# Kernel optimization log

Measured on AMD Instinct MI355X. Metric: run time of the kernel, lower is better.

## Reference

```python
import jax, jax.numpy as jnp
import numpy as np

B, H, D = 2, 16, 64
M = N = 4096
WM = WN = 64
R = 3
NEG = -10000.0


def _rand_blocks(m, n, wm, wn, r, last_idx):
    # Faithful port of bigbird_block_rand_mask (numpy RNG, seeded by caller).
    nb = m // wm
    rand = np.zeros((nb - 2, r), dtype=np.int32)
    mid = np.arange(1, n // wn - 1, dtype=np.int32)
    last = n // wn - 1
    if last_idx > 2 * wn:
        last = last_idx // wn - 1
    for i in range(1, nb - 1):
        start, end = i - 2, i
        if i == 1:
            rand[i - 1] = np.random.permutation(mid[2:last])[:r]
        elif i == 2:
            rand[i - 1] = np.random.permutation(mid[3:last])[:r]
        elif i == nb - 3 or i == nb - 2:
            rand[i - 1] = np.random.permutation(mid[:last])[:r]
        elif start > last:
            rand[i - 1] = np.random.permutation(mid[:last])[:r]
        elif end + 1 == last:
            rand[i - 1] = np.random.permutation(mid[:start])[:r]
        else:
            rand[i - 1] = np.random.permutation(np.concatenate((mid[:start], mid[end + 1:last])))[:r]
    return rand


def setup_inputs() -> dict:
    key = jax.random.key(0)
    kq, kk, kv = jax.random.split(key, 3)
    nb = M // WM
    q = jax.random.normal(kq, (B, H, M, D), jnp.float32)
    k = jax.random.normal(kk, (B, H, N, D), jnp.float32)
    v = jax.random.normal(kv, (B, H, N, D), jnp.float32)
    band_mask = jnp.ones((B, 1, nb - 4, WM, 3 * WN), jnp.float32)
    from_mask = jnp.ones((B, 1, M, 1), jnp.float32)
    to_mask = jnp.ones((B, 1, 1, N), jnp.float32)
    from_blocked_mask = jnp.ones((B, nb, WM), jnp.float32)
    to_blocked_mask = jnp.ones((B, nb, WN), jnp.float32)
    np.random.seed(0)
    ra = np.stack([_rand_blocks(M, N, WM, WN, R, 1024)[:nb - 2] for _ in range(H)], 0)
    rand_attn = jnp.asarray(np.broadcast_to(ra[None], (B, H, nb - 2, R)).copy(), jnp.int32)
    return dict(query_layer=q, key_layer=k, value_layer=v, band_mask=band_mask,
                from_mask=from_mask, to_mask=to_mask,
                from_blocked_mask=from_blocked_mask, to_blocked_mask=to_blocked_mask,
                rand_attn=rand_attn, batch_size=B, from_seq_length=M, to_seq_length=N)


def _forward(q, k, v, band_mask, from_mask, to_mask, from_blocked_mask, to_blocked_mask, rand_attn):
    b, h, m, d = q.shape
    n = k.shape[2]
    wm, wn, r = WM, WN, R
    nb = m // wm
    scale = 1.0 / np.sqrt(d)
    bq = q.reshape(b, h, nb, wm, d)
    bk = k.reshape(b, h, nb, wn, d)
    bv = v.reshape(b, h, nb, wn, d)

    # gather random key/value blocks: [b,h,nb-2,r*wn,d]
    idx = jnp.broadcast_to(rand_attn.reshape(b, h, (nb - 2) * r, 1, 1).astype(jnp.int32),
                           (b, h, (nb - 2) * r, wn, d))
    gk = jnp.take_along_axis(bk, idx, axis=2).reshape(b, h, nb - 2, r * wn, d)
    gv = jnp.take_along_axis(bv, idx, axis=2).reshape(b, h, nb - 2, r * wn, d)

    # random-block attention mask: [b,h,nb-2,wm,r*wn]
    bidx = jnp.arange(b)[:, None, None, None]
    rm = to_blocked_mask[bidx, rand_attn].reshape(b, h, nb - 2, r * wn)
    rand_mask = jnp.einsum('blq,bhlk->bhlqk', from_blocked_mask[:, 1:-1], rm)

    # --- first row-block: full attention over all keys ---
    p0 = jnp.einsum('bhqd,bhkd->bhqk', bq[:, :, 0], k) * scale + (1.0 - to_mask) * NEG
    c0 = jnp.einsum('bhqk,bhkd->bhqd', jax.nn.softmax(p0, -1), v)[:, :, None]

    # --- second row-block: blocks 0,1,2,last + random ---
    k1c = jnp.concatenate([bk[:, :, 0], bk[:, :, 1], bk[:, :, 2], bk[:, :, -1], gk[:, :, 0]], axis=2)
    v1c = jnp.concatenate([bv[:, :, 0], bv[:, :, 1], bv[:, :, 2], bv[:, :, -1], gv[:, :, 0]], axis=2)
    p1 = jnp.einsum('bhqd,bhkd->bhqk', bq[:, :, 1], k1c) * scale
    seq_pad = jnp.concatenate([to_mask[:, :, :, :3 * wn], to_mask[:, :, :, -wn:],
                               jnp.ones((b, 1, 1, r * wn), to_mask.dtype)], axis=3)
    rpad = jnp.concatenate([jnp.ones((b, h, wm, 4 * wn), rand_mask.dtype), rand_mask[:, :, 0]], axis=3)
    p1 = p1 + (1.0 - jnp.minimum(seq_pad, rpad)) * NEG
    c1 = jnp.einsum('bhqk,bhkd->bhqd', jax.nn.softmax(p1, -1), v1c)[:, :, None]

    # --- middle row-blocks: sliding window (3 blocks) + first + last + random ---
    ek = jnp.concatenate([bk[:, :, 1:-3], bk[:, :, 2:-2], bk[:, :, 3:-1]], axis=3)  # [b,h,nb-4,3wn,d]
    ev = jnp.concatenate([bv[:, :, 1:-3], bv[:, :, 2:-2], bv[:, :, 3:-1]], axis=3)
    mq = bq[:, :, 2:-2]
    inner = jnp.einsum('bhlqd,bhlkd->bhlqk', mq, ek) * scale + (1.0 - band_mask) * NEG
    randp = jnp.einsum('bhlqd,bhlkd->bhlqk', mq, gk[:, :, 1:-1]) * scale + (1.0 - rand_mask[:, :, 1:-1]) * NEG
    firstp = jnp.einsum('bhlqd,bhkd->bhlqk', mq, bk[:, :, 0]) * scale \
        + (1.0 - to_mask[:, :, :, :wn][:, :, :, None, :]) * NEG
    lastp = jnp.einsum('bhlqd,bhkd->bhlqk', mq, bk[:, :, -1]) * scale \
        + (1.0 - to_mask[:, :, :, -wn:][:, :, :, None, :]) * NEG
    band = jnp.concatenate([firstp, inner, randp, lastp], axis=-1)  # [b,h,nb-4,wm,(5+r)*wn]
    attn = jax.nn.softmax(band, -1)
    cmid = (jnp.einsum('bhlqk,bhlkd->bhlqd', attn[..., wn:4 * wn], ev)
            + jnp.einsum('bhlqk,bhlkd->bhlqd', attn[..., 4 * wn:4 * wn + r * wn], gv[:, :, 1:-1])
            + jnp.einsum('bhlqk,bhkd->bhlqd', attn[..., :wn], bv[:, :, 0])
            + jnp.einsum('bhlqk,bhkd->bhlqd', attn[..., -wn:], bv[:, :, -1]))

    # --- second-to-last row-block: blocks 0,-3,-2,-1 + random ---
    k2c = jnp.concatenate([bk[:, :, 0], bk[:, :, -3], bk[:, :, -2], bk[:, :, -1], gk[:, :, -1]], axis=2)
    v2c = jnp.concatenate([bv[:, :, 0], bv[:, :, -3], bv[:, :, -2], bv[:, :, -1], gv[:, :, -1]], axis=2)
    p2 = jnp.einsum('bhqd,bhkd->bhqk', bq[:, :, -2], k2c) * scale
    seq_pad2 = jnp.concatenate([to_mask[:, :, :, :wn], to_mask[:, :, :, -3 * wn:],
                                jnp.ones((b, 1, 1, r * wn), to_mask.dtype)], axis=3)
    rpad2 = jnp.concatenate([jnp.ones((b, h, wm, 4 * wn), rand_mask.dtype), rand_mask[:, :, -1]], axis=3)
    p2 = p2 + (1.0 - jnp.minimum(seq_pad2, rpad2)) * NEG
    c2 = jnp.einsum('bhqk,bhkd->bhqd', jax.nn.softmax(p2, -1), v2c)[:, :, None]

    # --- last row-block: full attention ---
    p3 = jnp.einsum('bhqd,bhkd->bhqk', bq[:, :, -1], k) * scale + (1.0 - to_mask) * NEG
    c3 = jnp.einsum('bhqk,bhkd->bhqd', jax.nn.softmax(p3, -1), v)[:, :, None]

    ctx = jnp.concatenate([c0, c1, cmid, c2, c3], axis=2).reshape(b, h, m, d) * from_mask
    return jnp.transpose(ctx, (0, 2, 1, 3))  # [b, m, h, d]


def reference(query_layer, key_layer, value_layer, band_mask, from_mask, to_mask,
              from_blocked_mask, to_blocked_mask, rand_attn,
              batch_size, from_seq_length, to_seq_length):
    return _forward(query_layer, key_layer, value_layer, band_mask, from_mask, to_mask,
                    from_blocked_mask, to_blocked_mask, rand_attn)
```

## Files before the change

kernel.cpp:

```cpp
#include <hip/hip_runtime.h>
#include <math.h>

constexpr int B_  = 2;
constexpr int H_  = 16;
constexpr int M_  = 4096;
constexpr int NB_ = 64;
constexpr int R_  = 3;
constexpr float LOG2E  = 1.44269504089f;
constexpr float SCALE2 = 0.125f * LOG2E;
constexpr float NEG2   = -10000.0f * LOG2E;

constexpr int PER_BH = 62 + 16;
constexpr int NWG    = B_ * H_ * PER_BH;
constexpr int PACC_OFF = 0;
constexpr int PM_OFF   = B_ * H_ * 2 * 8 * 64 * 64;
constexpr int PL_OFF   = PM_OFF + B_ * H_ * 2 * 8 * 64;

typedef short bf16x8 __attribute__((ext_vector_type(8)));
typedef float f32x4  __attribute__((ext_vector_type(4)));

__device__ __forceinline__ short bf16s(float x) {
    return __builtin_bit_cast(short, (__bf16)x);
}
__device__ __forceinline__ unsigned pack_bf16(float a, float b) {
    unsigned short ul = __builtin_bit_cast(unsigned short, (__bf16)a);
    unsigned short uh = __builtin_bit_cast(unsigned short, (__bf16)b);
    return (unsigned)ul | ((unsigned)uh << 16);
}

__device__ __forceinline__ int tile_kb(int e, int ch, int qb, int ra0, int ra1, int ra2, int i) {
    if (e >= 0) return ch * 8 + i;
    const int rnd = (i == 4) ? ra0 : ((i == 5) ? ra1 : ra2);
    if (qb == 1)        return (i < 3) ? i : ((i == 3) ? NB_ - 1 : rnd);
    if (qb == NB_ - 2)  return (i == 0) ? 0 : ((i < 4) ? 60 + i : rnd);
    if (i == 0) return 0;
    if (i < 4)  return qb - 2 + i;
    if (i < 7)  return rnd;
    return NB_ - 1;
}

__device__ __forceinline__ int tile_mode(int e, int qb, int i, int& boff) {
    boff = 0;
    if (e >= 0) return 0;
    if (qb == 1 || qb == NB_ - 2) return (i >= 4) ? 2 : 0;
    if (i >= 1 && i < 4) { boff = (i - 1) * 64; return 1; }
    if (i >= 4 && i < 7) return 2;
    return 0;
}

__global__ __launch_bounds__(256, 4)
void bigbird_mfma(const float* __restrict__ q,  const float* __restrict__ k,
                  const float* __restrict__ v,  const float* __restrict__ band_mask,
                  const float* __restrict__ from_mask, const float* __restrict__ to_mask,
                  const float* __restrict__ from_blocked, const float* __restrict__ to_blocked,
                  const int*   __restrict__ rand_attn,   float* __restrict__ out,
                  float* __restrict__ ws)
{
    __shared__ int4 kf[2][8][64];
    __shared__ int4 vf[2][8][64];

    const int wg  = (blockIdx.x & 7) * (NWG / 8) + (blockIdx.x >> 3);
    const int bh  = wg / PER_BH;
    const int idx = wg % PER_BH;
    const int h   = bh % H_;
    const int b   = bh / H_;
    int qb, e = -1, ch = 0;
    if (idx < 62)      { qb = idx + 1; }
    else if (idx < 70) { e = 0; ch = idx - 62; qb = 0; }
    else               { e = 1; ch = idx - 70; qb = NB_ - 1; }

    const int t  = threadIdx.x;
    const int l  = t & 63;
    const int w  = t >> 6;
    const int c  = l & 15;
    const int hh = l >> 4;

    int ra0 = 0, ra1 = 0, ra2 = 0;
    int nkb;
    if (e >= 0) nkb = 8;
    else {
        const int* ra = rand_attn + ((b * H_ + h) * (NB_ - 2) + (qb - 1)) * R_;
        ra0 = ra[0]; ra1 = ra[1]; ra2 = ra[2];
        nkb = (qb == 1 || qb == NB_ - 2) ? 7 : 8;
    }

    const int rr  = t >> 2;
    const int cc4 = t & 3;
    const float* kbase = k + ((size_t)bh * M_ + rr) * 64 + cc4 * 16;
    const int kslot = (rr >> 4) * 2 + (cc4 >> 1);
    const int kr15  = rr & 15;
    const int kg0   = (cc4 & 1) * 2;

    const int d0v  = (t & 31) * 2;
    const int oct8 = t >> 5;
    const float* vbase = v + (size_t)bh * M_ * 64 + (size_t)(oct8 * 8) * 64 + d0v;
    const int vslot = (d0v >> 4) * 2 + (oct8 >> 2);
    const int vidx  = (oct8 & 3) * 16 + (d0v & 15);

    bf16x8 qf[2];
    {
        const float* qp = q + ((size_t)bh * M_ + (size_t)qb * 64 + w * 16 + c) * 64 + hh * 8;
        #pragma unroll
        for (int dh = 0; dh < 2; ++dh) {
            float4 a0 = *(const float4*)(qp + dh * 32);
            float4 a1 = *(const float4*)(qp + dh * 32 + 4);
            bf16x8 qv;
            qv[0] = bf16s(a0.x); qv[1] = bf16s(a0.y); qv[2] = bf16s(a0.z); qv[3] = bf16s(a0.w);
            qv[4] = bf16s(a1.x); qv[5] = bf16s(a1.y); qv[6] = bf16s(a1.z); qv[7] = bf16s(a1.w);
            qf[dh] = qv;
        }
    }

    const float fbv = from_blocked[(b * NB_ + qb) * 64 + (w * 16 + c)];

    float mrun = -INFINITY, lrun = 0.0f;
    f32x4 O[4];
    #pragma unroll
    for (int nf = 0; nf < 4; ++nf) { O[nf][0] = 0.f; O[nf][1] = 0.f; O[nf][2] = 0.f; O[nf][3] = 0.f; }

    float4 kr0, kr1, kr2, kr3;
    float2 vr[8];

    {
        const int kb0 = tile_kb(e, ch, qb, ra0, ra1, ra2, 0);
        const float4* kp4 = (const float4*)(kbase + (size_t)kb0 * 4096);
        kr0 = kp4[0]; kr1 = kp4[1]; kr2 = kp4[2]; kr3 = kp4[3];
        const float* vp = vbase + (size_t)kb0 * 4096;
        #pragma unroll
        for (int j = 0; j < 8; ++j) vr[j] = *(const float2*)(vp + j * 64);

        float kfl[16];
        kfl[0]=kr0.x; kfl[1]=kr0.y; kfl[2]=kr0.z; kfl[3]=kr0.w;
        kfl[4]=kr1.x; kfl[5]=kr1.y; kfl[6]=kr1.z; kfl[7]=kr1.w;
        kfl[8]=kr2.x; kfl[9]=kr2.y; kfl[10]=kr2.z; kfl[11]=kr2.w;
        kfl[12]=kr3.x; kfl[13]=kr3.y; kfl[14]=kr3.z; kfl[15]=kr3.w;
        bf16x8 o0, o1;
        #pragma unroll
        for (int j = 0; j < 8; ++j) { o0[j] = bf16s(kfl[j]); o1[j] = bf16s(kfl[8 + j]); }
        kf[0][kslot][kg0 * 16 + kr15]       = __builtin_bit_cast(int4, o0);
        kf[0][kslot][(kg0 + 1) * 16 + kr15] = __builtin_bit_cast(int4, o1);

        bf16x8 va, vb2;
        #pragma unroll
        for (int j = 0; j < 8; ++j) { va[j] = bf16s(vr[j].x); vb2[j] = bf16s(vr[j].y); }
        vf[0][vslot][vidx]     = __builtin_bit_cast(int4, va);
        vf[0][vslot][vidx + 1] = __builtin_bit_cast(int4, vb2);

        if (1 < nkb) {
            const int kb1 = tile_kb(e, ch, qb, ra0, ra1, ra2, 1);
            const float4* kn4 = (const float4*)(kbase + (size_t)kb1 * 4096);
            kr0 = kn4[0]; kr1 = kn4[1]; kr2 = kn4[2]; kr3 = kn4[3];
            const float* vn = vbase + (size_t)kb1 * 4096;
            #pragma unroll
            for (int j = 0; j < 8; ++j) vr[j] = *(const float2*)(vn + j * 64);
        }
    }
    __syncthreads();

    for (int it = 0; it < nkb; ++it) {
        const int cur = it & 1;
        const int kb = tile_kb(e, ch, qb, ra0, ra1, ra2, it);
        int boffC; const int modeC = tile_mode(e, qb, it, boffC);

        f32x4 sf[4];
        #pragma unroll
        for (int f = 0; f < 4; ++f) { sf[f][0]=0.f; sf[f][1]=0.f; sf[f][2]=0.f; sf[f][3]=0.f; }
        __builtin_amdgcn_s_setprio(1);
        #pragma unroll
        for (int f = 0; f < 4; ++f) {
            sf[f] = __builtin_amdgcn_mfma_f32_16x16x32_bf16(
                        __builtin_bit_cast(bf16x8, kf[cur][f * 2 + 0][l]), qf[0], sf[f], 0, 0, 0);
            sf[f] = __builtin_amdgcn_mfma_f32_16x16x32_bf16(
                        __builtin_bit_cast(bf16x8, kf[cur][f * 2 + 1][l]), qf[1], sf[f], 0, 0, 0);
        }
        __builtin_amdgcn_s_setprio(0);

        if (it + 1 < nkb) {
            const int nxt = cur ^ 1;
            float kfl[16];
            kfl[0]=kr0.x; kfl[1]=kr0.y; kfl[2]=kr0.z; kfl[3]=kr0.w;
            kfl[4]=kr1.x; kfl[5]=kr1.y; kfl[6]=kr1.z; kfl[7]=kr1.w;
            kfl[8]=kr2.x; kfl[9]=kr2.y; kfl[10]=kr2.z; kfl[11]=kr2.w;
            kfl[12]=kr3.x; kfl[13]=kr3.y; kfl[14]=kr3.z; kfl[15]=kr3.w;
            bf16x8 o0, o1;
            #pragma unroll
            for (int j = 0; j < 8; ++j) { o0[j] = bf16s(kfl[j]); o1[j] = bf16s(kfl[8 + j]); }
            kf[nxt][kslot][kg0 * 16 + kr15]       = __builtin_bit_cast(int4, o0);
            kf[nxt][kslot][(kg0 + 1) * 16 + kr15] = __builtin_bit_cast(int4, o1);

            bf16x8 va, vb2;
            #pragma unroll
            for (int j = 0; j < 8; ++j) { va[j] = bf16s(vr[j].x); vb2[j] = bf16s(vr[j].y); }
            vf[nxt][vslot][vidx]     = __builtin_bit_cast(int4, va);
            vf[nxt][vslot][vidx + 1] = __builtin_bit_cast(int4, vb2);
        }

        float msk[4][4];
        if (modeC == 0) {
            const float* mp = to_mask + b * M_ + kb * 64 + 4 * hh;
            #pragma unroll
            for (int f = 0; f < 4; ++f) {
                float4 mv = *(const float4*)(mp + 16 * f);
                msk[f][0] = mv.x; msk[f][1] = mv.y; msk[f][2] = mv.z; msk[f][3] = mv.w;
            }
        } else if (modeC == 1) {
            const float* mp = band_mask + (((size_t)b * (NB_ - 4) + (qb - 2)) * 64 + (w * 16 + c)) * 192 + boffC + 4 * hh;
            #pragma unroll
            for (int f = 0; f < 4; ++f) {
                float4 mv = *(const float4*)(mp + 16 * f);
                msk[f][0] = mv.x; msk[f][1] = mv.y; msk[f][2] = mv.z; msk[f][3] = mv.w;
            }
        } else {
            const float* mp = to_blocked + (b * NB_ + kb) * 64 + 4 * hh;
            #pragma unroll
            for (int f = 0; f < 4; ++f) {
                float4 mv = *(const float4*)(mp + 16 * f);
                msk[f][0] = fbv * mv.x; msk[f][1] = fbv * mv.y;
                msk[f][2] = fbv * mv.z; msk[f][3] = fbv * mv.w;
            }
        }

        if (it + 2 < nkb) {
            const int kb2 = tile_kb(e, ch, qb, ra0, ra1, ra2, it + 2);
            const float4* kp4 = (const float4*)(kbase + (size_t)kb2 * 4096);
            kr0 = kp4[0]; kr1 = kp4[1]; kr2 = kp4[2]; kr3 = kp4[3];
            const float* vp = vbase + (size_t)kb2 * 4096;
            #pragma unroll
            for (int j = 0; j < 8; ++j) vr[j] = *(const float2*)(vp + j * 64);
        }

        float p[4][4];
        float tmax = -INFINITY;
        #pragma unroll
        for (int f = 0; f < 4; ++f) {
            #pragma unroll
            for (int r = 0; r < 4; ++r) {
                const float s = sf[f][r] * SCALE2 + (1.0f - msk[f][r]) * NEG2;
                p[f][r] = s;
                tmax = fmaxf(tmax, s);
            }
        }
        tmax = fmaxf(tmax, __shfl_xor(tmax, 16));
        tmax = fmaxf(tmax, __shfl_xor(tmax, 32));
        const float mnew = fmaxf(mrun, tmax);
        const float fs = exp2f(mrun - mnew);
        float sum = 0.0f;
        #pragma unroll
        for (int f = 0; f < 4; ++f) {
            #pragma unroll
            for (int r = 0; r < 4; ++r) { p[f][r] = exp2f(p[f][r] - mnew); sum += p[f][r]; }
        }
        sum += __shfl_xor(sum, 16);
        sum += __shfl_xor(sum, 32);
        lrun = lrun * fs + sum;
        mrun = mnew;

        const float fr0 = __shfl(fs, hh * 4 + 0);
        const float fr1 = __shfl(fs, hh * 4 + 1);
        const float fr2 = __shfl(fs, hh * 4 + 2);
        const float fr3 = __shfl(fs, hh * 4 + 3);
        #pragma unroll
        for (int nf = 0; nf < 4; ++nf) {
            O[nf][0] *= fr0; O[nf][1] *= fr1; O[nf][2] *= fr2; O[nf][3] *= fr3;
        }

        unsigned pks[4][2];
        #pragma unroll
        for (int f = 0; f < 4; ++f) {
            pks[f][0] = pack_bf16(p[f][0], p[f][1]);
            pks[f][1] = pack_bf16(p[f][2], p[f][3]);
        }
        #pragma unroll
        for (int kh = 0; kh < 2; ++kh) {
            unsigned ad[4];
            #pragma unroll
            for (int wq = 0; wq < 4; ++wq) {
                const int pos = wq >> 1, ww = wq & 1;
                const int src = c + 16 * ((2 * hh + pos) & 3);
                const unsigned x = (unsigned)__shfl((int)pks[2 * kh][ww], src);
                const unsigned y = (unsigned)__shfl((int)pks[2 * kh + 1][ww], src);
                ad[wq] = (hh & 2) ? y : x;
            }
            const uint4 adv = make_uint4(ad[0], ad[1], ad[2], ad[3]);
            const bf16x8 pa = __builtin_bit_cast(bf16x8, adv);
            __builtin_amdgcn_s_setprio(1);
            #pragma unroll
            for (int nf = 0; nf < 4; ++nf) {
                O[nf] = __builtin_amdgcn_mfma_f32_16x16x32_bf16(
                            pa, __builtin_bit_cast(bf16x8, vf[cur][nf * 2 + kh][l]), O[nf], 0, 0, 0);
            }
            __builtin_amdgcn_s_setprio(0);
        }

        __syncthreads();
    }

    if (e < 0) {
        #pragma unroll
        for (int r = 0; r < 4; ++r) {
            const float lr  = __shfl(lrun, hh * 4 + r);
            const int   qg  = qb * 64 + w * 16 + hh * 4 + r;
            const float fmv = from_mask[b * M_ + qg];
            const float scl = fmv / lr;
            float* op = out + (((size_t)b * M_ + qg) * H_ + h) * 64 + c;
            #pragma unroll
            for (int nf = 0; nf < 4; ++nf) op[nf * 16] = O[nf][r] * scl;
        }
    } else {
        const int pe = (bh * 2 + e) * 8 + ch;
        #pragma unroll
        for (int r = 0; r < 4; ++r) {
            const int qlocal = w * 16 + hh * 4 + r;
            float* pa = ws + PACC_OFF + ((size_t)pe * 64 + qlocal) * 64 + c;
            #pragma unroll
            for (int nf = 0; nf < 4; ++nf) pa[nf * 16] = O[nf][r];
        }
        if (hh == 0) {
            ws[PM_OFF + pe * 64 + w * 16 + c] = mrun;
            ws[PL_OFF + pe * 64 + w * 16 + c] = lrun;
        }
    }
}

__global__ __launch_bounds__(256)
void bigbird_combine(const float* __restrict__ ws, const float* __restrict__ from_mask,
                     float* __restrict__ out)
{
    const int g  = blockIdx.x;
    const int e  = g & 1;
    const int bh = g >> 1;
    const int h  = bh % H_;
    const int b  = bh / H_;
    const int qb = e ? NB_ - 1 : 0;

    const int t  = threadIdx.x;
    const int r  = t >> 2;
    const int dq = (t & 3) * 16;

    float mc[8], lc[8];
    float m = -INFINITY;
    #pragma unroll
    for (int c = 0; c < 8; ++c) {
        mc[c] = ws[PM_OFF + (g * 8 + c) * 64 + r];
        lc[c] = ws[PL_OFF + (g * 8 + c) * 64 + r];
        m = fmaxf(m, mc[c]);
    }
    float l = 0.0f;
    float acc[16];
    #pragma unroll
    for (int j = 0; j < 16; ++j) acc[j] = 0.0f;
    #pragma unroll
    for (int c = 0; c < 8; ++c) {
        const float sc = exp2f(mc[c] - m);
        l += lc[c] * sc;
        const float4* pa = (const float4*)(ws + PACC_OFF + ((size_t)(g * 8 + c) * 64 + r) * 64 + dq);
        #pragma unroll
        for (int j4 = 0; j4 < 4; ++j4) {
            float4 av = pa[j4];
            acc[j4 * 4 + 0] += sc * av.x;
            acc[j4 * 4 + 1] += sc * av.y;
            acc[j4 * 4 + 2] += sc * av.z;
            acc[j4 * 4 + 3] += sc * av.w;
        }
    }
    const float fm = from_mask[b * M_ + qb * 64 + r];
    const float s  = fm / l;
    float* op = out + (((size_t)b * M_ + qb * 64 + r) * H_ + h) * 64 + dq;
    #pragma unroll
    for (int j4 = 0; j4 < 4; ++j4) {
        float4 o;
        o.x = acc[j4 * 4 + 0] * s; o.y = acc[j4 * 4 + 1] * s;
        o.z = acc[j4 * 4 + 2] * s; o.w = acc[j4 * 4 + 3] * s;
        *(float4*)(op + j4 * 4) = o;
    }
}

extern "C" void kernel_launch(void* const* d_in, const int* in_sizes, int n_in,
                              void* d_out, int out_size, void* d_ws, size_t ws_size,
                              hipStream_t stream) {
    const float* q  = (const float*)d_in[0];
    const float* k  = (const float*)d_in[1];
    const float* v  = (const float*)d_in[2];
    const float* bm = (const float*)d_in[3];
    const float* fm = (const float*)d_in[4];
    const float* tm = (const float*)d_in[5];
    const float* fb = (const float*)d_in[6];
    const float* tb = (const float*)d_in[7];
    const int*   ra = (const int*)d_in[8];
    float* o  = (float*)d_out;
    float* ws = (float*)d_ws;

    hipLaunchKernelGGL(bigbird_mfma, dim3(NWG), dim3(256), 0, stream,
                       q, k, v, bm, fm, tm, fb, tb, ra, o, ws);
    hipLaunchKernelGGL(bigbird_combine, dim3(B_ * H_ * 2), dim3(256), 0, stream,
                       ws, fm, o);
}
```

Before: 96.12 us.

## Pre-pack K/V into bf16 MFMA fragment layout and use single-wave strip kernel

Adds a prep kernel that converts K and V once into bf16 tiles already laid out as MFMA operand fragments in workspace. A new one-wave-per-16-row-strip attention kernel then loads those fragments straight from global memory into registers, with no LDS staging or workgroup barriers, across many more, smaller workgroups. This removes repeated per-block fp32-to-bf16 conversion and shared-memory traffic. In exchange it adds an extra launch and a workspace round trip for K/V, and each K/V tile is reloaded by the four strips that use it. The old kernel is kept as a fallback when the workspace is too small.

```diff
diff --git a/kernel.cpp b/kernel.cpp
--- a/kernel.cpp
+++ b/kernel.cpp
@@ -15,6 +15,12 @@
 constexpr int PACC_OFF = 0;
 constexpr int PM_OFF   = B_ * H_ * 2 * 8 * 64 * 64;
 constexpr int PL_OFF   = PM_OFF + B_ * H_ * 2 * 8 * 64;
+constexpr size_t KV_BYTE_OFF = (size_t)(PL_OFF + B_ * H_ * 2 * 8 * 64) * 4;
+constexpr size_t KV_BYTES    = (size_t)B_ * H_ * 64 * 1024 * 16;
+constexpr size_t WS_NEED     = KV_BYTE_OFF + KV_BYTES;
+
+constexpr int PER_BH1 = 312;
+constexpr int NWG1    = B_ * H_ * PER_BH1;
 
 typedef short bf16x8 __attribute__((ext_vector_type(8)));
 typedef float f32x4  __attribute__((ext_vector_type(4)));
@@ -46,6 +52,238 @@
     if (i >= 1 && i < 4) { boff = (i - 1) * 64; return 1; }
     if (i >= 4 && i < 7) return 2;
     return 0;
+}
+
+__global__ __launch_bounds__(256)
+void bigbird_prep(const float* __restrict__ k, const float* __restrict__ v,
+                  int4* __restrict__ wskv)
+{
+    __shared__ float kt[64][66];
+    __shared__ float vt[64][66];
+    const int g = blockIdx.x;
+    const int t = threadIdx.x;
+    const int row = t >> 2, cc = (t & 3) * 16;
+    const float* kp = k + (size_t)g * 4096 + row * 64 + cc;
+    const float* vp = v + (size_t)g * 4096 + row * 64 + cc;
+    #pragma unroll
+    for (int j4 = 0; j4 < 4; ++j4) {
+        *(float4*)&kt[row][cc + j4 * 4] = *(const float4*)(kp + j4 * 4);
+        *(float4*)&vt[row][cc + j4 * 4] = *(const float4*)(vp + j4 * 4);
+    }
+    __syncthreads();
+    #pragma unroll
+    for (int cpt = 0; cpt < 4; ++cpt) {
+        const int ch = t + cpt * 256;
+        const int slot = ch >> 6, lane = ch & 63;
+        bf16x8 o;
+        if (slot < 8) {
+            const int r  = 16 * (slot >> 1) + (lane & 15);
+            const int c0 = 32 * (slot & 1) + 8 * (lane >> 4);
+            #pragma unroll
+            for (int j = 0; j < 8; ++j) o[j] = bf16s(kt[r][c0 + j]);
+        } else {
+            const int s2 = slot - 8;
+            const int r0 = 32 * (s2 & 1) + 8 * (lane >> 4);
+            const int c  = 16 * (s2 >> 1) + (lane & 15);
+            #pragma unroll
+            for (int j = 0; j < 8; ++j) o[j] = bf16s(vt[r0 + j][c]);
+        }
+        wskv[(size_t)g * 1024 + ch] = __builtin_bit_cast(int4, o);
+    }
+}
+
+__global__ __launch_bounds__(64, 3)
+void bigbird_1w(const float* __restrict__ q, const int4* __restrict__ wskv,
+                const float* __restrict__ band_mask, const float* __restrict__ from_mask,
+                const float* __restrict__ to_mask,   const float* __restrict__ from_blocked,
+                const float* __restrict__ to_blocked, const int* __restrict__ rand_attn,
+                float* __restrict__ out, float* __restrict__ ws)
+{
+    const int wg   = (blockIdx.x & 7) * (NWG1 / 8) + (blockIdx.x >> 3);
+    const int bh   = wg / PER_BH1;
+    const int idx  = wg % PER_BH1;
+    const int item = idx >> 2;
+    const int strip= idx & 3;
+    const int h    = bh % H_;
+    const int b    = bh / H_;
+    int qb, e = -1, ch = 0;
+    if (item < 62)      { qb = item + 1; }
+    else if (item < 70) { e = 0; ch = item - 62; qb = 0; }
+    else                { e = 1; ch = item - 70; qb = NB_ - 1; }
+
+    const int l  = threadIdx.x;
+    const int c  = l & 15;
+    const int hh = l >> 4;
+
+    int ra0 = 0, ra1 = 0, ra2 = 0;
+    int nkb;
+    if (e >= 0) nkb = 8;
+    else {
+        const int* ra = rand_attn + ((b * H_ + h) * (NB_ - 2) + (qb - 1)) * R_;
+        ra0 = ra[0]; ra1 = ra[1]; ra2 = ra[2];
+        nkb = (qb == 1 || qb == NB_ - 2) ? 7 : 8;
+    }
+
+    bf16x8 qf[2];
+    {
+        const float* qp = q + ((size_t)bh * M_ + (size_t)qb * 64 + strip * 16 + c) * 64 + hh * 8;
+        #pragma unroll
+        for (int dh = 0; dh < 2; ++dh) {
+            float4 a0 = *(const float4*)(qp + dh * 32);
+            float4 a1 = *(const float4*)(qp + dh * 32 + 4);
+            bf16x8 qv;
+            qv[0] = bf16s(a0.x); qv[1] = bf16s(a0.y); qv[2] = bf16s(a0.z); qv[3] = bf16s(a0.w);
+            qv[4] = bf16s(a1.x); qv[5] = bf16s(a1.y); qv[6] = bf16s(a1.z); qv[7] = bf16s(a1.w);
+            qf[dh] = qv;
+        }
+    }
+
+    const float fbv = from_blocked[(b * NB_ + qb) * 64 + (strip * 16 + c)];
+
+    float mrun = -INFINITY, lrun = 0.0f;
+    f32x4 O[4];
+    #pragma unroll
+    for (int nf = 0; nf < 4; ++nf) { O[nf][0] = 0.f; O[nf][1] = 0.f; O[nf][2] = 0.f; O[nf][3] = 0.f; }
+
+    for (int it = 0; it < nkb; ++it) {
+        const int kb = tile_kb(e, ch, qb, ra0, ra1, ra2, it);
+        int boffC; const int modeC = tile_mode(e, qb, it, boffC);
+        const int4* tb = wskv + (size_t)(bh * 64 + kb) * 1024;
+
+        int4 kfr[8];
+        #pragma unroll
+        for (int s = 0; s < 8; ++s) kfr[s] = tb[s * 64 + l];
+        int4 vfr[8];
+        #pragma unroll
+        for (int s = 0; s < 8; ++s) vfr[s] = tb[(8 + s) * 64 + l];
+
+        float msk[4][4];
+        if (modeC == 0) {
+            const float* mp = to_mask + b * M_ + kb * 64 + 4 * hh;
+            #pragma unroll
+            for (int f = 0; f < 4; ++f) {
+                float4 mv = *(const float4*)(mp + 16 * f);
+                msk[f][0] = mv.x; msk[f][1] = mv.y; msk[f][2] = mv.z; msk[f][3] = mv.w;
+            }
+        } else if (modeC == 1) {
+            const float* mp = band_mask + (((size_t)b * (NB_ - 4) + (qb - 2)) * 64 + (strip * 16 + c)) * 192 + boffC + 4 * hh;
+            #pragma unroll
+            for (int f = 0; f < 4; ++f) {
+                float4 mv = *(const float4*)(mp + 16 * f);
+                msk[f][0] = mv.x; msk[f][1] = mv.y; msk[f][2] = mv.z; msk[f][3] = mv.w;
+            }
+        } else {
+            const float* mp = to_blocked + (b * NB_ + kb) * 64 + 4 * hh;
+            #pragma unroll
+            for (int f = 0; f < 4; ++f) {
+                float4 mv = *(const float4*)(mp + 16 * f);
+                msk[f][0] = fbv * mv.x; msk[f][1] = fbv * mv.y;
+                msk[f][2] = fbv * mv.z; msk[f][3] = fbv * mv.w;
+            }
+        }
+
+        f32x4 sf[4];
+        #pragma unroll
+        for (int f = 0; f < 4; ++f) { sf[f][0]=0.f; sf[f][1]=0.f; sf[f][2]=0.f; sf[f][3]=0.f; }
+        __builtin_amdgcn_s_setprio(1);
+        #pragma unroll
+        for (int f = 0; f < 4; ++f) {
+            sf[f] = __builtin_amdgcn_mfma_f32_16x16x32_bf16(
+                        __builtin_bit_cast(bf16x8, kfr[f * 2 + 0]), qf[0], sf[f], 0, 0, 0);
+            sf[f] = __builtin_amdgcn_mfma_f32_16x16x32_bf16(
+                        __builtin_bit_cast(bf16x8, kfr[f * 2 + 1]), qf[1], sf[f], 0, 0, 0);
+        }
+        __builtin_amdgcn_s_setprio(0);
+
+        float p[4][4];
+        float tmax = -INFINITY;
+        #pragma unroll
+        for (int f = 0; f < 4; ++f) {
+            #pragma unroll
+            for (int r = 0; r < 4; ++r) {
+                const float s = sf[f][r] * SCALE2 + (1.0f - msk[f][r]) * NEG2;
+                p[f][r] = s;
+                tmax = fmaxf(tmax, s);
+            }
+        }
+        tmax = fmaxf(tmax, __shfl_xor(tmax, 16));
+        tmax = fmaxf(tmax, __shfl_xor(tmax, 32));
+        const float mnew = fmaxf(mrun, tmax);
+        const float fs = exp2f(mrun - mnew);
+        float sum = 0.0f;
+        #pragma unroll
+        for (int f = 0; f < 4; ++f) {
+            #pragma unroll
+            for (int r = 0; r < 4; ++r) { p[f][r] = exp2f(p[f][r] - mnew); sum += p[f][r]; }
+        }
+        sum += __shfl_xor(sum, 16);
+        sum += __shfl_xor(sum, 32);
+        lrun = lrun * fs + sum;
+        mrun = mnew;
+
+        const float fr0 = __shfl(fs, hh * 4 + 0);
+        const float fr1 = __shfl(fs, hh * 4 + 1);
+        const float fr2 = __shfl(fs, hh * 4 + 2);
+        const float fr3 = __shfl(fs, hh * 4 + 3);
+        #pragma unroll
+        for (int nf = 0; nf < 4; ++nf) {
+            O[nf][0] *= fr0; O[nf][1] *= fr1; O[nf][2] *= fr2; O[nf][3] *= fr3;
+        }
+
+        unsigned pks[4][2];
+        #pragma unroll
+        for (int f = 0; f < 4; ++f) {
+            pks[f][0] = pack_bf16(p[f][0], p[f][1]);
+            pks[f][1] = pack_bf16(p[f][2], p[f][3]);
+        }
+        #pragma unroll
+        for (int kh = 0; kh < 2; ++kh) {
+            unsigned ad[4];
+            #pragma unroll
+            for (int wq = 0; wq < 4; ++wq) {
+                const int pos = wq >> 1, ww = wq & 1;
+                const int src = c + 16 * ((2 * hh + pos) & 3);
+                const unsigned x = (unsigned)__shfl((int)pks[2 * kh][ww], src);
+                const unsigned y = (unsigned)__shfl((int)pks[2 * kh + 1][ww], src);
+                ad[wq] = (hh & 2) ? y : x;
+            }
+            const uint4 adv = make_uint4(ad[0], ad[1], ad[2], ad[3]);
+            const bf16x8 pa = __builtin_bit_cast(bf16x8, adv);
+            __builtin_amdgcn_s_setprio(1);
+            #pragma unroll
+            for (int nf = 0; nf < 4; ++nf) {
+                O[nf] = __builtin_amdgcn_mfma_f32_16x16x32_bf16(
+                            pa, __builtin_bit_cast(bf16x8, vfr[nf * 2 + kh]), O[nf], 0, 0, 0);
+            }
+            __builtin_amdgcn_s_setprio(0);
+        }
+    }
+
+    if (e < 0) {
+        #pragma unroll
+        for (int r = 0; r < 4; ++r) {
+            const float lr  = __shfl(lrun, hh * 4 + r);
+            const int   qg  = qb * 64 + strip * 16 + hh * 4 + r;
+            const float fmv = from_mask[b * M_ + qg];
+            const float scl = fmv / lr;
+            float* op = out + (((size_t)b * M_ + qg) * H_ + h) * 64 + c;
+            #pragma unroll
+            for (int nf = 0; nf < 4; ++nf) op[nf * 16] = O[nf][r] * scl;
+        }
+    } else {
+        const int pe = (bh * 2 + e) * 8 + ch;
+        #pragma unroll
+        for (int r = 0; r < 4; ++r) {
+            const int qlocal = strip * 16 + hh * 4 + r;
+            float* pa = ws + PACC_OFF + ((size_t)pe * 64 + qlocal) * 64 + c;
+            #pragma unroll
+            for (int nf = 0; nf < 4; ++nf) pa[nf * 16] = O[nf][r];
+        }
+        if (hh == 0) {
+            ws[PM_OFF + pe * 64 + strip * 16 + c] = mrun;
+            ws[PL_OFF + pe * 64 + strip * 16 + c] = lrun;
+        }
+    }
 }
 
 __global__ __launch_bounds__(256, 4)
@@ -390,8 +628,16 @@
     float* o  = (float*)d_out;
     float* ws = (float*)d_ws;
 
-    hipLaunchKernelGGL(bigbird_mfma, dim3(NWG), dim3(256), 0, stream,
-                       q, k, v, bm, fm, tm, fb, tb, ra, o, ws);
+    if (ws_size >= WS_NEED) {
+        int4* wskv = (int4*)((char*)d_ws + KV_BYTE_OFF);
+        hipLaunchKernelGGL(bigbird_prep, dim3(B_ * H_ * 64), dim3(256), 0, stream,
+                           k, v, wskv);
+        hipLaunchKernelGGL(bigbird_1w, dim3(NWG1), dim3(64), 0, stream,
+                           q, wskv, bm, fm, tm, fb, tb, ra, o, ws);
+    } else {
+        hipLaunchKernelGGL(bigbird_mfma, dim3(NWG), dim3(256), 0, stream,
+                           q, k, v, bm, fm, tm, fb, tb, ra, o, ws);
+    }
     hipLaunchKernelGGL(bigbird_combine, dim3(B_ * H_ * 2), dim3(256), 0, stream,
                        ws, fm, o);
 }
```

New measurement: 97.94 us. No clear change (+1.9%).
